# Kernel tuning notes

Hardware: AMD Instinct MI355X
Metric: run time of the kernel (lower is better)

## Reference

```python
import jax, jax.numpy as jnp
import numpy as np

N_PROT, N_LIG = 8192, 2048
E_PP, E_LP = 163840, 81920
D_NODE, D_EDGE, D_CHI = 128, 128, 64
H, DH = 4, 32            # num_attention_heads, head dim (H*DH == D_NODE)
HD = H * DH
D_SRC_PP = 2 * D_NODE + D_EDGE + D_CHI      # 448, pre-expanded pp source feats
Z0 = D_SRC_PP + D_NODE                      # pp edge: [src_exp || prot_sink], edge dim 0
Z1 = 3 * D_NODE                             # lp edge: [lig_src || prot_sink || eattr]
D_FF = 4 * D_NODE


def _ln(x, g, b):
    m = x.mean(-1, keepdims=True)
    v = x.var(-1, keepdims=True)
    return (x - m) / jnp.sqrt(v + 1e-5) * g + b


def _seg_softmax(logits, seg, n):
    # logits: [E, H]; softmax over edges sharing the same sink node
    m = jax.ops.segment_max(logits, seg, num_segments=n)
    e = jnp.exp(logits - m[seg])
    s = jax.ops.segment_sum(e, seg, num_segments=n)
    return e / (s[seg] + 1e-9)


def setup_inputs() -> dict:
    key = jax.random.key(0)
    ks = jax.random.split(key, 32)
    p = lambda k, shape, fan: jax.random.normal(k, shape, jnp.float32) / np.sqrt(fan)
    inp = {
        "source_node_edge_features_exp": jax.random.normal(ks[0], (E_PP, D_SRC_PP), jnp.float32),
        "prot_scalars": jax.random.normal(ks[1], (N_PROT, D_NODE), jnp.float32),
        "prot_vectors": jax.random.normal(ks[2], (N_PROT, 4, 3), jnp.float32),
        "pr_pr_edge_index": jax.random.randint(ks[3], (2, E_PP), 0, N_PROT),
        "lig_scalars": jax.random.normal(ks[4], (N_LIG, D_NODE), jnp.float32),
        "lig_pr_eattr": jax.random.normal(ks[5], (E_LP, D_EDGE), jnp.float32),
        "lig_pr_edge_index": jax.random.randint(ks[6], (2, E_LP), 0, N_LIG),
        # per-edge-type GATv2 weights (subgraph 0 = prot-prot, 1 = lig-prot)
        "Watt0": p(ks[7], (Z0, HD), Z0), "batt0": jnp.zeros((HD,), jnp.float32),
        "a0": p(ks[8], (H, DH), DH),
        "Wval0": p(ks[9], (Z0, HD), Z0), "bval0": jnp.zeros((HD,), jnp.float32),
        "Watt1": p(ks[10], (Z1, HD), Z1), "batt1": jnp.zeros((HD,), jnp.float32),
        "a1": p(ks[11], (H, DH), DH),
        "Wval1": p(ks[12], (Z1, HD), Z1), "bval1": jnp.zeros((HD,), jnp.float32),
        # attention-head aggregation MLP (atten_head_aggr_layers = 2)
        "Wh1": p(ks[13], (HD, HD), HD), "bh1": jnp.zeros((HD,), jnp.float32),
        "Wh2": p(ks[14], (HD, D_NODE), HD), "bh2": jnp.zeros((D_NODE,), jnp.float32),
        "ln1_g": jnp.ones((D_NODE,), jnp.float32), "ln1_b": jnp.zeros((D_NODE,), jnp.float32),
        # residual node-update MLP
        "Wm1": p(ks[15], (D_NODE, D_FF), D_NODE), "bm1": jnp.zeros((D_FF,), jnp.float32),
        "Wm2": p(ks[16], (D_FF, D_NODE), D_FF), "bm2": jnp.zeros((D_NODE,), jnp.float32),
        "ln2_g": jnp.ones((D_NODE,), jnp.float32), "ln2_b": jnp.zeros((D_NODE,), jnp.float32),
    }
    return inp


def reference(source_node_edge_features_exp, prot_scalars, prot_vectors,
              pr_pr_edge_index, lig_scalars, lig_pr_eattr, lig_pr_edge_index,
              Watt0, batt0, a0, Wval0, bval0,
              Watt1, batt1, a1, Wval1, bval1,
              Wh1, bh1, Wh2, bh2, ln1_g, ln1_b,
              Wm1, bm1, Wm2, bm2, ln2_g, ln2_b):
    n = prot_scalars.shape[0]

    def gat(z, sink, Watt, batt, a, Wval, bval):
        e = z.shape[0]
        h = (z @ Watt + batt).reshape(e, H, DH)
        logit = jnp.einsum('ehd,hd->eh', jax.nn.leaky_relu(h, 0.2), a)  # GATv2 scoring
        alpha = _seg_softmax(logit, sink, n)
        v = (z @ Wval + bval).reshape(e, H, DH)
        return jax.ops.segment_sum((v * alpha[..., None]).reshape(e, HD), sink, num_segments=n)

    # gather source/sink features per edge set (pp edges already pre-expanded, edge dim 0)
    z0 = jnp.concatenate([source_node_edge_features_exp, prot_scalars[pr_pr_edge_index[1]]], axis=-1)
    z1 = jnp.concatenate([lig_scalars[lig_pr_edge_index[0]],
                          prot_scalars[lig_pr_edge_index[1]], lig_pr_eattr], axis=-1)
    attn = gat(z0, pr_pr_edge_index[1], Watt0, batt0, a0, Wval0, bval0) \
         + gat(z1, lig_pr_edge_index[1], Watt1, batt1, a1, Wval1, bval1)
    attn = jax.nn.gelu(attn @ Wh1 + bh1) @ Wh2 + bh2       # head aggregation MLP
    x = _ln(prot_scalars + attn, ln1_g, ln1_b)             # residual node update
    x = _ln(x + jax.nn.gelu(x @ Wm1 + bm1) @ Wm2 + bm2, ln2_g, ln2_b)
    return x, prot_vectors  # EquivariantData: updated scalars, vectors pass through
```

## Files before the change

### kernel.cpp

```cpp
#include <hip/hip_runtime.h>

#define N_PROT 8192
#define E_PP   163840
#define E_LP   81920
#define NB0    (E_PP / 64)
#define NB1    (E_LP / 64)
#define XSTR   132

typedef float        f32x2  __attribute__((ext_vector_type(2)));
typedef float        f32x4  __attribute__((ext_vector_type(4)));
typedef float        f32x16 __attribute__((ext_vector_type(16)));
typedef unsigned int u32x2  __attribute__((ext_vector_type(2)));
typedef unsigned int u32x4  __attribute__((ext_vector_type(4)));
typedef short        s16x8  __attribute__((ext_vector_type(8)));
typedef unsigned short ushort_t;

union frag32 { u32x4 v; s16x8 s; };

__device__ inline unsigned short f2bf(float f) {
  unsigned int u = __float_as_uint(f);
  u = u + 0x7FFFu + ((u >> 16) & 1u);
  return (unsigned short)(u >> 16);
}

__device__ inline unsigned int cvt_pk_bf16(float lo, float hi) {
  unsigned int r;
  asm("v_cvt_pk_bf16_f32 %0, %1, %2" : "=v"(r) : "v"(lo), "v"(hi));
  return r;
}

__device__ inline float bf_lo(unsigned int u) { return __uint_as_float(u << 16); }
__device__ inline float bf_hi(unsigned int u) { return __uint_as_float(u & 0xffff0000u); }

__device__ inline float gelu_tanh(float x) {
  const float c0 = 0.7978845608028654f;
  float inner = c0 * (x + 0.044715f * x * x * x);
  return 0.5f * x * (1.0f + tanhf(inner));
}

__global__ void build_bt(const float* __restrict__ Watt, const float* __restrict__ Wval,
                         ushort_t* __restrict__ Bt, int K)
{
  int i = blockIdx.x * 256 + threadIdx.x;
  if (i >= K * 256) return;
  int k = i >> 8, n = i & 255;
  float v = (n < 128) ? Watt[(size_t)k * 128 + n] : Wval[(size_t)k * 128 + (n - 128)];
  Bt[(size_t)(k >> 3) * 2048 + n * 8 + (k & 7)] = f2bf(v);
}

__global__ void build_wt(const float* __restrict__ W, ushort_t* __restrict__ Wt,
                         int total, int shift)
{
  int i = blockIdx.x * 256 + threadIdx.x;
  if (i >= total) return;
  int k = i >> shift, n = i & ((1 << shift) - 1);
  Wt[(size_t)(k >> 3) * (8 << shift) + n * 8 + (k & 7)] = f2bf(W[i]);
}

__global__ void build_perm(const float* __restrict__ batt0, const float* __restrict__ a0,
                           const float* __restrict__ bval0,
                           const float* __restrict__ batt1, const float* __restrict__ a1,
                           const float* __restrict__ bval1,
                           float* __restrict__ P)
{
  const int t = threadIdx.x;
  const int m = t / 384;
  const int r = t % 384;
  const float* batt = m ? batt1 : batt0;
  const float* avec = m ? a1 : a0;
  const float* bval = m ? bval1 : bval0;
  float* base = P + m * 384;
  if (r < 256) {
    const int h = r >> 6, hi = (r >> 5) & 1, q = (r >> 1) & 15, c = r & 1;
    const int rq = (q & 3) + 8 * (q >> 2) + 4 * hi;
    base[r] = c ? avec[h * 32 + rq] : batt[h * 32 + rq];
  } else {
    const int i = r - 256;
    const int g = i >> 5, hi = (i >> 4) & 1, q = i & 15;
    const int rq = (q & 3) + 8 * (q >> 2) + 4 * hi;
    base[256 + i] = bval[g * 32 + rq];
  }
}

__global__ void csr_hist(const int* __restrict__ e0, const int* __restrict__ e1,
                         int* __restrict__ cnt0, int* __restrict__ cnt1)
{
  const int i = blockIdx.x * 256 + threadIdx.x;
  if (i < E_PP) atomicAdd(&cnt0[e0[E_PP + i]], 1);
  if (i < E_LP) atomicAdd(&cnt1[e1[E_LP + i]], 1);
}

__global__ void csr_scan2(const int* __restrict__ cnt0, int* __restrict__ off0,
                          const int* __restrict__ cnt1, int* __restrict__ off1)
{
  const int* cnt = blockIdx.x ? cnt1 : cnt0;
  int* off = blockIdx.x ? off1 : off0;
  __shared__ int ps[1024];
  const int t = threadIdx.x;
  int loc[8];
  int s = 0;
  #pragma unroll
  for (int i = 0; i < 8; ++i) { loc[i] = cnt[t * 8 + i]; s += loc[i]; }
  ps[t] = s;
  __syncthreads();
  for (int d = 1; d < 1024; d <<= 1) {
    int v = (t >= d) ? ps[t - d] : 0;
    __syncthreads();
    ps[t] += v;
    __syncthreads();
  }
  int ex = ps[t] - s;
  #pragma unroll
  for (int i = 0; i < 8; ++i) { off[t * 8 + i] = ex; ex += loc[i]; }
  if (t == 1023) off[8192] = ps[1023];
}

__global__ void csr_scat(const int* __restrict__ e0, const int* __restrict__ e1,
                         const int* __restrict__ off0, const int* __restrict__ off1,
                         int* __restrict__ cur0, int* __restrict__ cur1,
                         int* __restrict__ pel0, int* __restrict__ pel1)
{
  const int i = blockIdx.x * 256 + threadIdx.x;
  if (i < E_PP) { int s = e0[E_PP + i]; pel0[i] = off0[s] + atomicAdd(&cur0[s], 1); }
  if (i < E_LP) { int s = e1[E_LP + i]; pel1[i] = off1[s] + atomicAdd(&cur1[s], 1); }
}

template<int MODE>
__device__ __forceinline__ void edge_body(
    int blk, char* AsmS, char* BsmS, f32x4* epsLds,
    const float* __restrict__ Afeat, const float* __restrict__ prot,
    const float* __restrict__ eattr, const int* __restrict__ eidx,
    const int* __restrict__ pel,
    const ushort_t* __restrict__ Bt, const float* __restrict__ P,
    char* __restrict__ ev, float* __restrict__ eb)
{
  constexpr int K  = (MODE == 0) ? 576 : 384;
  constexpr int E  = (MODE == 0) ? E_PP : E_LP;
  constexpr int NT = K / 16;

  const int t    = threadIdx.x;
  const int lane = t & 63;
  const int w    = t >> 6;
  const int gl   = w >> 1;
  const int role = w & 1;
  const int col  = lane & 31;
  const int hi   = lane >> 5;
  const int eid  = blk * 64 + gl * 32 + col;
  const int pos  = pel[eid];

  const int srow = t >> 2;
  const int sq   = t & 3;
  const int seid = blk * 64 + srow;
  const int ssnk = eidx[E + seid];
  const float* sA;
  const float* sP;
  const float* sE = nullptr;
  if (MODE == 0) {
    sA = Afeat + (size_t)seid * 448 + sq * 4;
    sP = prot  + (size_t)ssnk * 128 + sq * 4;
  } else {
    sA = Afeat + (size_t)eidx[seid] * 128 + sq * 4;
    sP = prot  + (size_t)ssnk * 128 + sq * 4;
    sE = eattr + (size_t)seid * 128 + sq * 4;
  }
  auto sptr = [&](int s) -> const float* {
    const int k0 = s * 16;
    if (MODE == 0) return (k0 < 448) ? (sA + k0) : (sP + (k0 - 448));
    const int r = k0 >> 7, kk = k0 & 127;
    return (r == 0) ? (sA + kk) : (r == 1) ? (sP + kk) : (sE + kk);
  };
  char* const wrA = AsmS + (srow >> 5) * 1536 + (srow & 31) * 48 + sq * 8;
  const char* const rdA = AsmS + gl * 1536 + col * 48 + hi * 16;

  const u32x4* btv = (const u32x4*)Bt;
  char* const wrB = BsmS + t * 32;
  const char* const rdB = BsmS + role * 2048 + hi * 4096 + col * 16;

  f32x16 acc[4];
  #pragma unroll
  for (int i = 0; i < 4; ++i) acc[i] = (f32x16)(0.0f);

  f32x4 gA1, gA2;
  u32x4 gB1a, gB1b, gB2a, gB2b;
  {
    f32x4 g0 = *(const f32x4*)sptr(0);
    u32x4 b0a = btv[t * 2], b0b = btv[t * 2 + 1];
    gA1  = *(const f32x4*)sptr(1);
    gB1a = btv[512 + t * 2];
    gB1b = btv[512 + t * 2 + 1];
    u32x2 pk;
    pk.x = cvt_pk_bf16(g0.x, g0.y);
    pk.y = cvt_pk_bf16(g0.z, g0.w);
    *(u32x2*)wrA = pk;
    u32x4* wb = (u32x4*)wrB;
    wb[0] = b0a; wb[1] = b0b;
  }
  __syncthreads();

  #pragma unroll
  for (int s = 0; s < NT; ++s) {
    const int p = s & 1;
    if (s + 2 < NT) {
      gA2  = *(const f32x4*)sptr(s + 2);
      gB2a = btv[(size_t)(s + 2) * 512 + t * 2];
      gB2b = btv[(size_t)(s + 2) * 512 + t * 2 + 1];
    }

    frag32 af;
    af.v = *(const u32x4*)(rdA + p * 3072);
    const char* bs = rdB + p * 8192;
    #pragma unroll
    for (int nbl = 0; nbl < 4; ++nbl) {
      frag32 bf;
      bf.v = *(const u32x4*)(bs + nbl * 512);
      acc[nbl] = __builtin_amdgcn_mfma_f32_32x32x16_bf16(bf.s, af.s, acc[nbl], 0, 0, 0);
    }

    if (s + 1 < NT) {
      u32x2 pk;
      pk.x = cvt_pk_bf16(gA1.x, gA1.y);
      pk.y = cvt_pk_bf16(gA1.z, gA1.w);
      *(u32x2*)(wrA + (p ^ 1) * 3072) = pk;
      u32x4* wb = (u32x4*)(wrB + (p ^ 1) * 8192);
      wb[0] = gB1a; wb[1] = gB1b;
    }
    gA1 = gA2; gB1a = gB2a; gB1b = gB2b;
    asm volatile("s_waitcnt lgkmcnt(0)\n\ts_barrier" ::: "memory");
  }

  if (role == 0) {
    float ep[4];
    #pragma unroll
    for (int h = 0; h < 4; ++h) {
      const f32x4* tp = (const f32x4*)(P + (h * 2 + hi) * 32);
      float partial = 0.f;
      #pragma unroll
      for (int q = 0; q < 16; q += 2) {
        const f32x4 ba = tp[q >> 1];
        float x0 = acc[h][q]     + ba.x; x0 = (x0 > 0.f) ? x0 : 0.2f * x0;
        float x1 = acc[h][q + 1] + ba.z; x1 = (x1 > 0.f) ? x1 : 0.2f * x1;
        partial = fmaf(x0, ba.y, partial);
        partial = fmaf(x1, ba.w, partial);
      }
      const float full = partial + __shfl_xor(partial, 32, 64);
      ep[h] = __expf(full);
    }
    f32x2 ef2;
    ef2.x = hi ? ep[2] : ep[0];
    ef2.y = hi ? ep[3] : ep[1];
    *(f32x2*)(eb + (size_t)pos * 4 + 2 * hi) = ef2;
    if (hi == 0) {
      f32x4 ef = {ep[0], ep[1], ep[2], ep[3]};
      epsLds[gl * 32 + col] = ef;
    }
  }
  __syncthreads();
  if (role == 1) {
    const f32x4 ep4 = epsLds[gl * 32 + col];
    const float* bvp = P + 256;
    char* row = ev + (size_t)pos * 256;
    #pragma unroll
    for (int g = 0; g < 4; ++g) {
      const float wgt = ep4[g];
      const float* bv = bvp + (g * 2 + hi) * 16;
      #pragma unroll
      for (int s = 0; s < 4; ++s) {
        const float v0 = (acc[g][s * 4 + 0] + bv[s * 4 + 0]) * wgt;
        const float v1 = (acc[g][s * 4 + 1] + bv[s * 4 + 1]) * wgt;
        const float v2 = (acc[g][s * 4 + 2] + bv[s * 4 + 2]) * wgt;
        const float v3 = (acc[g][s * 4 + 3] + bv[s * 4 + 3]) * wgt;
        u32x2 pk;
        pk.x = cvt_pk_bf16(v0, v1);
        pk.y = cvt_pk_bf16(v2, v3);
        *(u32x2*)(row + g * 64 + s * 16 + hi * 8) = pk;
      }
    }
  }
}

__global__ __launch_bounds__(256, 3)
void edge_gat10(const float* __restrict__ src_exp, const float* __restrict__ prot,
                const float* __restrict__ lig, const float* __restrict__ eattr,
                const int* __restrict__ eidx0, const int* __restrict__ eidx1,
                const int* __restrict__ pel0, const int* __restrict__ pel1,
                const ushort_t* __restrict__ Bt0, const ushort_t* __restrict__ Bt1,
                const float* __restrict__ P,
                char* __restrict__ ev0, float* __restrict__ eb0,
                char* __restrict__ ev1, float* __restrict__ eb1)
{
  __shared__ alignas(16) char AsmS[2 * 3072];
  __shared__ alignas(16) char BsmS[2 * 8192];
  __shared__ f32x4 eps[64];
  const int bid = blockIdx.x;
  if (bid < NB0)
    edge_body<0>(bid, AsmS, BsmS, eps, src_exp, prot, nullptr, eidx0, pel0,
                 Bt0, P, ev0, eb0);
  else
    edge_body<1>(bid - NB0, AsmS, BsmS, eps, lig, prot, eattr, eidx1, pel1,
                 Bt1, P + 384, ev1, eb1);
}

__device__ inline void ln_rows16(const float* __restrict__ src, int ss,
                                 float* __restrict__ dst, int ds,
                                 const float* __restrict__ g, const float* __restrict__ b,
                                 const int t)
{
  const int lane = t & 63;
  const int n    = (t >> 6) * 4 + (lane >> 4);
  const int c0   = (lane & 15) * 8;
  f32x4 va = *(const f32x4*)&src[n * ss + c0];
  f32x4 vb = *(const f32x4*)&src[n * ss + c0 + 4];
  float s = va.x + va.y + va.z + va.w + vb.x + vb.y + vb.z + vb.w;
  float q = va.x * va.x + va.y * va.y + va.z * va.z + va.w * va.w
          + vb.x * vb.x + vb.y * vb.y + vb.z * vb.z + vb.w * vb.w;
  #pragma unroll
  for (int m = 1; m < 16; m <<= 1) {
    s += __shfl_xor(s, m, 64);
    q += __shfl_xor(q, m, 64);
  }
  const float mean = s * 0.0078125f;
  const float var  = q * 0.0078125f - mean * mean;
  const float r    = rsqrtf(var + 1e-5f);
  f32x4 oa, ob;
  oa.x = (va.x - mean) * r * g[c0 + 0] + b[c0 + 0];
  oa.y = (va.y - mean) * r * g[c0 + 1] + b[c0 + 1];
  oa.z = (va.z - mean) * r * g[c0 + 2] + b[c0 + 2];
  oa.w = (va.w - mean) * r * g[c0 + 3] + b[c0 + 3];
  ob.x = (vb.x - mean) * r * g[c0 + 4] + b[c0 + 4];
  ob.y = (vb.y - mean) * r * g[c0 + 5] + b[c0 + 5];
  ob.z = (vb.z - mean) * r * g[c0 + 6] + b[c0 + 6];
  ob.w = (vb.w - mean) * r * g[c0 + 7] + b[c0 + 7];
  *(f32x4*)&dst[n * ds + c0]     = oa;
  *(f32x4*)&dst[n * ds + c0 + 4] = ob;
}

__global__ __launch_bounds__(256, 2)
void node_mfma(const int* __restrict__ off0, const char* __restrict__ ev0,
               const float* __restrict__ eb0,
               const int* __restrict__ off1, const char* __restrict__ ev1,
               const float* __restrict__ eb1,
               const float* __restrict__ prot,
               const ushort_t* __restrict__ Wh1t, const float* __restrict__ bh1,
               const ushort_t* __restrict__ Wh2t, const float* __restrict__ bh2,
               const float* __restrict__ ln1g, const float* __restrict__ ln1b,
               const ushort_t* __restrict__ Wm1t, const float* __restrict__ bm1,
               const ushort_t* __restrict__ Wm2t, const float* __restrict__ bm2,
               const float* __restrict__ ln2g, const float* __restrict__ ln2b,
               float* __restrict__ out)
{
  __shared__ alignas(16) char xA[8 * 1536];
  __shared__ alignas(16) char r2[32 * XSTR * 4];
  const int t    = threadIdx.x;
  const int lane = t & 63;
  const int w    = t >> 6;
  const int l31  = lane & 31;
  const int hi   = lane >> 5;
  const int m0   = blockIdx.x * 32;
  float* xs = (float*)r2;
  char*  t3A = r2;

  #pragma unroll
  for (int it = 0; it < 2; ++it) {
    const int u  = t + it * 256;
    const int nl = u >> 4, j = u & 15;
    const int n  = m0 + nl;
    float va0[8] = {0,0,0,0,0,0,0,0}, va1[8] = {0,0,0,0,0,0,0,0};
    float d0v = 0.f, d1v = 0.f;
    {
      const int end = off0[n + 1];
      for (int itr = off0[n]; itr < end; ++itr) {
        const u32x4 r = *(const u32x4*)(ev0 + (size_t)itr * 256 + j * 16);
        d0v += eb0[(size_t)itr * 4 + (j >> 2)];
        #pragma unroll
        for (int i = 0; i < 4; ++i) {
          va0[2 * i]     += bf_lo(r[i]);
          va0[2 * i + 1] += bf_hi(r[i]);
        }
      }
    }
    {
      const int end = off1[n + 1];
      for (int itr = off1[n]; itr < end; ++itr) {
        const u32x4 r = *(const u32x4*)(ev1 + (size_t)itr * 256 + j * 16);
        d1v += eb1[(size_t)itr * 4 + (j >> 2)];
        #pragma unroll
        for (int i = 0; i < 4; ++i) {
          va1[2 * i]     += bf_lo(r[i]);
          va1[2 * i + 1] += bf_hi(r[i]);
        }
      }
    }
    const float inv0 = 1.f / (d0v + 1e-9f);
    const float inv1 = 1.f / (d1v + 1e-9f);
    float res[8];
    #pragma unroll
    for (int i = 0; i < 8; ++i) res[i] = va0[i] * inv0 + va1[i] * inv1;
    u32x4 pk;
    pk.x = cvt_pk_bf16(res[0], res[1]);
    pk.y = cvt_pk_bf16(res[2], res[3]);
    pk.z = cvt_pk_bf16(res[4], res[5]);
    pk.w = cvt_pk_bf16(res[6], res[7]);
    *(u32x4*)(xA + (j >> 1) * 1536 + nl * 48 + (j & 1) * 16) = pk;
  }
  __syncthreads();

  const char* rdA = xA + l31 * 48 + hi * 16;
  f32x16 acc;

  acc = (f32x16)(0.0f);
  #pragma unroll
  for (int s = 0; s < 8; ++s) {
    frag32 af, bf;
    af.v = *(const u32x4*)(rdA + s * 1536);
    bf.v = *(const u32x4*)((const char*)Wh1t + (2 * s + hi) * 2048 + (w * 32 + l31) * 16);
    acc = __builtin_amdgcn_mfma_f32_32x32x16_bf16(bf.s, af.s, acc, 0, 0, 0);
  }
  __syncthreads();
  #pragma unroll
  for (int jr = 0; jr < 4; ++jr) {
    const int c0 = w * 32 + jr * 8 + 4 * hi;
    const f32x4 bb = *(const f32x4*)(bh1 + c0);
    const float v0 = gelu_tanh(acc[4 * jr + 0] + bb.x);
    const float v1 = gelu_tanh(acc[4 * jr + 1] + bb.y);
    const float v2 = gelu_tanh(acc[4 * jr + 2] + bb.z);
    const float v3 = gelu_tanh(acc[4 * jr + 3] + bb.w);
    u32x2 pk;
    pk.x = cvt_pk_bf16(v0, v1);
    pk.y = cvt_pk_bf16(v2, v3);
    *(u32x2*)(xA + (c0 >> 4) * 1536 + l31 * 48 + ((c0 >> 3) & 1) * 16 + (c0 & 7) * 2) = pk;
  }
  __syncthreads();

  acc = (f32x16)(0.0f);
  #pragma unroll
  for (int s = 0; s < 8; ++s) {
    frag32 af, bf;
    af.v = *(const u32x4*)(rdA + s * 1536);
    bf.v = *(const u32x4*)((const char*)Wh2t + (2 * s + hi) * 2048 + (w * 32 + l31) * 16);
    acc = __builtin_amdgcn_mfma_f32_32x32x16_bf16(bf.s, af.s, acc, 0, 0, 0);
  }
  __syncthreads();
  #pragma unroll
  for (int q = 0; q < 16; ++q) {
    const int col = w * 32 + (q & 3) + 8 * (q >> 2) + 4 * hi;
    xs[l31 * XSTR + col] = acc[q];
  }
  __syncthreads();
  #pragma unroll
  for (int it = 0; it < 4; ++it) {
    const int u = t + it * 256;
    const int row = u >> 5, c4 = (u & 31) * 4;
    f32x4 v = *(f32x4*)&xs[row * XSTR + c4];
    const f32x4 p = *(const f32x4*)&prot[(size_t)(m0 + row) * 128 + c4];
    const f32x4 b = *(const f32x4*)&bh2[c4];
    v += p + b;
    *(f32x4*)&xs[row * XSTR + c4] = v;
  }
  __syncthreads();
  ln_rows16(xs, XSTR, xs, XSTR, ln1g, ln1b, t);
  ln_rows16(xs + 16 * XSTR, XSTR, xs + 16 * XSTR, XSTR, ln1g, ln1b, t);
  __syncthreads();
  #pragma unroll
  for (int it = 0; it < 4; ++it) {
    const int u = t + it * 256;
    const int row = u >> 5, c4 = (u & 31) * 4;
    const f32x4 v = *(const f32x4*)&xs[row * XSTR + c4];
    u32x2 pk;
    pk.x = cvt_pk_bf16(v.x, v.y);
    pk.y = cvt_pk_bf16(v.z, v.w);
    *(u32x2*)(xA + (c4 >> 4) * 1536 + row * 48 + ((c4 >> 3) & 1) * 16 + (c4 & 7) * 2) = pk;
  }
  __syncthreads();

  f32x16 acc5 = (f32x16)(0.0f);
  for (int ch = 0; ch < 4; ++ch) {
    f32x16 a4 = (f32x16)(0.0f);
    #pragma unroll
    for (int s = 0; s < 8; ++s) {
      frag32 af, bf;
      af.v = *(const u32x4*)(rdA + s * 1536);
      bf.v = *(const u32x4*)((const char*)Wm1t + (2 * s + hi) * 8192
                             + (ch * 128 + w * 32 + l31) * 16);
      a4 = __builtin_amdgcn_mfma_f32_32x32x16_bf16(bf.s, af.s, a4, 0, 0, 0);
    }
    __syncthreads();
    #pragma unroll
    for (int jr = 0; jr < 4; ++jr) {
      const int c0 = w * 32 + jr * 8 + 4 * hi;
      const f32x4 bb = *(const f32x4*)(bm1 + ch * 128 + c0);
      const float v0 = gelu_tanh(a4[4 * jr + 0] + bb.x);
      const float v1 = gelu_tanh(a4[4 * jr + 1] + bb.y);
      const float v2 = gelu_tanh(a4[4 * jr + 2] + bb.z);
      const float v3 = gelu_tanh(a4[4 * jr + 3] + bb.w);
      u32x2 pk;
      pk.x = cvt_pk_bf16(v0, v1);
      pk.y = cvt_pk_bf16(v2, v3);
      *(u32x2*)(t3A + (c0 >> 4) * 1536 + l31 * 48 + ((c0 >> 3) & 1) * 16 + (c0 & 7) * 2) = pk;
    }
    __syncthreads();
    #pragma unroll
    for (int s = 0; s < 8; ++s) {
      frag32 af, bf;
      af.v = *(const u32x4*)(t3A + s * 1536 + l31 * 48 + hi * 16);
      bf.v = *(const u32x4*)((const char*)Wm2t + (ch * 16 + 2 * s + hi) * 2048
                             + (w * 32 + l31) * 16);
      acc5 = __builtin_amdgcn_mfma_f32_32x32x16_bf16(bf.s, af.s, acc5, 0, 0, 0);
    }
    __syncthreads();
  }

  #pragma unroll
  for (int q = 0; q < 16; ++q) {
    const int col = w * 32 + (q & 3) + 8 * (q >> 2) + 4 * hi;
    xs[l31 * XSTR + col] = acc5[q];
  }
  __syncthreads();
  #pragma unroll
  for (int it = 0; it < 4; ++it) {
    const int u = t + it * 256;
    const int row = u >> 5, c4 = (u & 31) * 4;
    f32x4 v = *(f32x4*)&xs[row * XSTR + c4];
    const u32x2 xx = *(const u32x2*)(xA + (c4 >> 4) * 1536 + row * 48
                                     + ((c4 >> 3) & 1) * 16 + (c4 & 7) * 2);
    const f32x4 b = *(const f32x4*)&bm2[c4];
    v.x += bf_lo(xx.x) + b.x;
    v.y += bf_hi(xx.x) + b.y;
    v.z += bf_lo(xx.y) + b.z;
    v.w += bf_hi(xx.y) + b.w;
    *(f32x4*)&xs[row * XSTR + c4] = v;
  }
  __syncthreads();
  ln_rows16(xs, XSTR, out + (size_t)m0 * 128, 128, ln2g, ln2b, t);
  ln_rows16(xs + 16 * XSTR, XSTR, out + (size_t)(m0 + 16) * 128, 128, ln2g, ln2b, t);
}

extern "C" void kernel_launch(void* const* d_in, const int* in_sizes, int n_in,
                              void* d_out, int out_size, void* d_ws, size_t ws_size,
                              hipStream_t stream)
{
  const float* src_exp = (const float*)d_in[0];
  const float* prot    = (const float*)d_in[1];
  const float* pvec    = (const float*)d_in[2];
  const int*   eidx0   = (const int*)d_in[3];
  const float* lig     = (const float*)d_in[4];
  const float* eattr   = (const float*)d_in[5];
  const int*   eidx1   = (const int*)d_in[6];
  const float* Watt0 = (const float*)d_in[7];
  const float* batt0 = (const float*)d_in[8];
  const float* a0    = (const float*)d_in[9];
  const float* Wval0 = (const float*)d_in[10];
  const float* bval0 = (const float*)d_in[11];
  const float* Watt1 = (const float*)d_in[12];
  const float* batt1 = (const float*)d_in[13];
  const float* a1    = (const float*)d_in[14];
  const float* Wval1 = (const float*)d_in[15];
  const float* bval1 = (const float*)d_in[16];
  const float* Wh1  = (const float*)d_in[17];
  const float* bh1  = (const float*)d_in[18];
  const float* Wh2  = (const float*)d_in[19];
  const float* bh2  = (const float*)d_in[20];
  const float* ln1g = (const float*)d_in[21];
  const float* ln1b = (const float*)d_in[22];
  const float* Wm1  = (const float*)d_in[23];
  const float* bm1  = (const float*)d_in[24];
  const float* Wm2  = (const float*)d_in[25];
  const float* bm2  = (const float*)d_in[26];
  const float* ln2g = (const float*)d_in[27];
  const float* ln2b = (const float*)d_in[28];

  char* w = (char*)d_ws;
  size_t o = 0;
  auto take = [&](size_t b) -> void* {
    void* p = w + o;
    o += (b + 255) & ~(size_t)255;
    return p;
  };
  int* cnt0 = (int*)take(8192 * 4);
  int* cnt1 = (int*)take(8192 * 4);
  int* cur0 = (int*)take(8192 * 4);
  int* cur1 = (int*)take(8192 * 4);
  int* off0 = (int*)take(8193 * 4);
  int* off1 = (int*)take(8193 * 4);
  int* pel0 = (int*)take((size_t)E_PP * 4);
  int* pel1 = (int*)take((size_t)E_LP * 4);
  ushort_t* Bt0 = (ushort_t*)take((size_t)576 * 256 * 2);
  ushort_t* Bt1 = (ushort_t*)take((size_t)384 * 256 * 2);
  ushort_t* Wh1t = (ushort_t*)take((size_t)128 * 128 * 2);
  ushort_t* Wh2t = (ushort_t*)take((size_t)128 * 128 * 2);
  ushort_t* Wm1t = (ushort_t*)take((size_t)128 * 512 * 2);
  ushort_t* Wm2t = (ushort_t*)take((size_t)512 * 128 * 2);
  float* P = (float*)take(768 * 4);
  char*  ev0 = (char*)take((size_t)E_PP * 256);
  char*  ev1 = (char*)take((size_t)E_LP * 256);
  float* eb0 = (float*)take((size_t)E_PP * 16);
  float* eb1 = (float*)take((size_t)E_LP * 16);

  build_bt<<<(576 * 256) / 256, 256, 0, stream>>>(Watt0, Wval0, Bt0, 576);
  build_bt<<<(384 * 256) / 256, 256, 0, stream>>>(Watt1, Wval1, Bt1, 384);
  build_wt<<<64, 256, 0, stream>>>(Wh1, Wh1t, 128 * 128, 7);
  build_wt<<<64, 256, 0, stream>>>(Wh2, Wh2t, 128 * 128, 7);
  build_wt<<<256, 256, 0, stream>>>(Wm1, Wm1t, 128 * 512, 9);
  build_wt<<<256, 256, 0, stream>>>(Wm2, Wm2t, 512 * 128, 7);
  build_perm<<<1, 768, 0, stream>>>(batt0, a0, bval0, batt1, a1, bval1, P);

  hipMemsetAsync(cnt0, 0, 4 * 8192 * 4, stream);
  csr_hist<<<E_PP / 256, 256, 0, stream>>>(eidx0, eidx1, cnt0, cnt1);
  csr_scan2<<<2, 1024, 0, stream>>>(cnt0, off0, cnt1, off1);
  csr_scat<<<E_PP / 256, 256, 0, stream>>>(eidx0, eidx1, off0, off1,
                                           cur0, cur1, pel0, pel1);

  edge_gat10<<<NB0 + NB1, 256, 0, stream>>>(
      src_exp, prot, lig, eattr, eidx0, eidx1, pel0, pel1, Bt0, Bt1, P,
      ev0, eb0, ev1, eb1);

  node_mfma<<<N_PROT / 32, 256, 0, stream>>>(
      off0, ev0, eb0, off1, ev1, eb1, prot,
      Wh1t, bh1, Wh2t, bh2, ln1g, ln1b,
      Wm1t, bm1, Wm2t, bm2, ln2g, ln2b, (float*)d_out);

  hipMemcpyAsync((float*)d_out + (size_t)N_PROT * 128, pvec,
                 (size_t)N_PROT * 12 * sizeof(float), hipMemcpyDeviceToDevice, stream);
}
```

Measured before the change: 289.9 us.

## Split segment gather into a separate high-occupancy kernel and merge prep launches

Moves the per-node CSR aggregation of edge values out of the node MLP kernel into a new seg_gather kernel with 1024 blocks, each node handled by 32 threads that split the edge list in two and combine the halves through shared memory. The result is stored as a bf16 attention buffer that node_mfma then reads. All weight-transposition kernels, the bias permutation and the memset are folded into one prep_all launch to cut launch overhead. The cost is an extra kernel launch and a round trip to global memory for the intermediate buffer.

New measurement: 258.1 us. 11.0% less time.

```diff
diff --git a/kernel.cpp b/kernel.cpp
--- a/kernel.cpp
+++ b/kernel.cpp
@@ -38,47 +38,90 @@
   return 0.5f * x * (1.0f + tanhf(inner));
 }
 
-__global__ void build_bt(const float* __restrict__ Watt, const float* __restrict__ Wval,
-                         ushort_t* __restrict__ Bt, int K)
-{
-  int i = blockIdx.x * 256 + threadIdx.x;
-  if (i >= K * 256) return;
-  int k = i >> 8, n = i & 255;
-  float v = (n < 128) ? Watt[(size_t)k * 128 + n] : Wval[(size_t)k * 128 + (n - 128)];
-  Bt[(size_t)(k >> 3) * 2048 + n * 8 + (k & 7)] = f2bf(v);
-}
-
-__global__ void build_wt(const float* __restrict__ W, ushort_t* __restrict__ Wt,
-                         int total, int shift)
-{
-  int i = blockIdx.x * 256 + threadIdx.x;
-  if (i >= total) return;
-  int k = i >> shift, n = i & ((1 << shift) - 1);
-  Wt[(size_t)(k >> 3) * (8 << shift) + n * 8 + (k & 7)] = f2bf(W[i]);
-}
-
-__global__ void build_perm(const float* __restrict__ batt0, const float* __restrict__ a0,
-                           const float* __restrict__ bval0,
-                           const float* __restrict__ batt1, const float* __restrict__ a1,
-                           const float* __restrict__ bval1,
-                           float* __restrict__ P)
-{
+__global__ void prep_all(const float* __restrict__ Watt0, const float* __restrict__ Wval0,
+                         const float* __restrict__ Watt1, const float* __restrict__ Wval1,
+                         const float* __restrict__ Wh1, const float* __restrict__ Wh2,
+                         const float* __restrict__ Wm1, const float* __restrict__ Wm2,
+                         const float* __restrict__ batt0, const float* __restrict__ a0,
+                         const float* __restrict__ bval0,
+                         const float* __restrict__ batt1, const float* __restrict__ a1,
+                         const float* __restrict__ bval1,
+                         ushort_t* __restrict__ Bt0, ushort_t* __restrict__ Bt1,
+                         ushort_t* __restrict__ Wh1t, ushort_t* __restrict__ Wh2t,
+                         ushort_t* __restrict__ Wm1t, ushort_t* __restrict__ Wm2t,
+                         float* __restrict__ P, int* __restrict__ zbuf)
+{
+  int b = blockIdx.x;
   const int t = threadIdx.x;
-  const int m = t / 384;
-  const int r = t % 384;
-  const float* batt = m ? batt1 : batt0;
-  const float* avec = m ? a1 : a0;
-  const float* bval = m ? bval1 : bval0;
-  float* base = P + m * 384;
-  if (r < 256) {
-    const int h = r >> 6, hi = (r >> 5) & 1, q = (r >> 1) & 15, c = r & 1;
-    const int rq = (q & 3) + 8 * (q >> 2) + 4 * hi;
-    base[r] = c ? avec[h * 32 + rq] : batt[h * 32 + rq];
-  } else {
-    const int i = r - 256;
-    const int g = i >> 5, hi = (i >> 4) & 1, q = i & 15;
-    const int rq = (q & 3) + 8 * (q >> 2) + 4 * hi;
-    base[256 + i] = bval[g * 32 + rq];
+  if (b < 576) {
+    const int i = b * 256 + t;
+    const int k = i >> 8, n = i & 255;
+    const float v = (n < 128) ? Watt0[(size_t)k * 128 + n] : Wval0[(size_t)k * 128 + (n - 128)];
+    Bt0[(size_t)(k >> 3) * 2048 + n * 8 + (k & 7)] = f2bf(v);
+    return;
+  }
+  b -= 576;
+  if (b < 384) {
+    const int i = b * 256 + t;
+    const int k = i >> 8, n = i & 255;
+    const float v = (n < 128) ? Watt1[(size_t)k * 128 + n] : Wval1[(size_t)k * 128 + (n - 128)];
+    Bt1[(size_t)(k >> 3) * 2048 + n * 8 + (k & 7)] = f2bf(v);
+    return;
+  }
+  b -= 384;
+  if (b < 64) {
+    const int i = b * 256 + t;
+    const int k = i >> 7, n = i & 127;
+    Wh1t[(size_t)(k >> 3) * 1024 + n * 8 + (k & 7)] = f2bf(Wh1[i]);
+    return;
+  }
+  b -= 64;
+  if (b < 64) {
+    const int i = b * 256 + t;
+    const int k = i >> 7, n = i & 127;
+    Wh2t[(size_t)(k >> 3) * 1024 + n * 8 + (k & 7)] = f2bf(Wh2[i]);
+    return;
+  }
+  b -= 64;
+  if (b < 256) {
+    const int i = b * 256 + t;
+    const int k = i >> 9, n = i & 511;
+    Wm1t[(size_t)(k >> 3) * 4096 + n * 8 + (k & 7)] = f2bf(Wm1[i]);
+    return;
+  }
+  b -= 256;
+  if (b < 256) {
+    const int i = b * 256 + t;
+    const int k = i >> 7, n = i & 127;
+    Wm2t[(size_t)(k >> 3) * 1024 + n * 8 + (k & 7)] = f2bf(Wm2[i]);
+    return;
+  }
+  b -= 256;
+  if (b < 3) {
+    const int u = b * 256 + t;
+    if (u >= 768) return;
+    const int m = u / 384;
+    const int r = u % 384;
+    const float* batt = m ? batt1 : batt0;
+    const float* avec = m ? a1 : a0;
+    const float* bval = m ? bval1 : bval0;
+    float* base = P + m * 384;
+    if (r < 256) {
+      const int h = r >> 6, hi = (r >> 5) & 1, q = (r >> 1) & 15, c = r & 1;
+      const int rq = (q & 3) + 8 * (q >> 2) + 4 * hi;
+      base[r] = c ? avec[h * 32 + rq] : batt[h * 32 + rq];
+    } else {
+      const int i = r - 256;
+      const int g = i >> 5, hi = (i >> 4) & 1, q = i & 15;
+      const int rq = (q & 3) + 8 * (q >> 2) + 4 * hi;
+      base[256 + i] = bval[g * 32 + rq];
+    }
+    return;
+  }
+  b -= 3;
+  {
+    const int i = b * 256 + t;
+    if (i < 32768) zbuf[i] = 0;
   }
 }
 
@@ -300,6 +343,71 @@
                  Bt1, P + 384, ev1, eb1);
 }
 
+__global__ __launch_bounds__(256)
+void seg_gather(const int* __restrict__ off0, const char* __restrict__ ev0,
+                const float* __restrict__ eb0,
+                const int* __restrict__ off1, const char* __restrict__ ev1,
+                const float* __restrict__ eb1,
+                ushort_t* __restrict__ att)
+{
+  __shared__ float xch[8 * 16 * 18];
+  const int t    = threadIdx.x;
+  const int nl   = t >> 5;
+  const int half = (t >> 4) & 1;
+  const int j    = t & 15;
+  const int n    = blockIdx.x * 8 + nl;
+
+  float va0[8] = {0,0,0,0,0,0,0,0}, va1[8] = {0,0,0,0,0,0,0,0};
+  float d0 = 0.f, d1 = 0.f;
+  {
+    const int end = off0[n + 1];
+    for (int it = off0[n] + half; it < end; it += 2) {
+      const u32x4 r = *(const u32x4*)(ev0 + (size_t)it * 256 + j * 16);
+      d0 += eb0[(size_t)it * 4 + (j >> 2)];
+      #pragma unroll
+      for (int i = 0; i < 4; ++i) {
+        va0[2 * i]     += bf_lo(r[i]);
+        va0[2 * i + 1] += bf_hi(r[i]);
+      }
+    }
+  }
+  {
+    const int end = off1[n + 1];
+    for (int it = off1[n] + half; it < end; it += 2) {
+      const u32x4 r = *(const u32x4*)(ev1 + (size_t)it * 256 + j * 16);
+      d1 += eb1[(size_t)it * 4 + (j >> 2)];
+      #pragma unroll
+      for (int i = 0; i < 4; ++i) {
+        va1[2 * i]     += bf_lo(r[i]);
+        va1[2 * i + 1] += bf_hi(r[i]);
+      }
+    }
+  }
+  float* slot = xch + (nl * 16 + j) * 18;
+  if (half) {
+    #pragma unroll
+    for (int i = 0; i < 8; ++i) { slot[i] = va0[i]; slot[8 + i] = va1[i]; }
+    slot[16] = d0; slot[17] = d1;
+  }
+  __syncthreads();
+  if (!half) {
+    #pragma unroll
+    for (int i = 0; i < 8; ++i) { va0[i] += slot[i]; va1[i] += slot[8 + i]; }
+    d0 += slot[16]; d1 += slot[17];
+    const float inv0 = 1.f / (d0 + 1e-9f);
+    const float inv1 = 1.f / (d1 + 1e-9f);
+    float res[8];
+    #pragma unroll
+    for (int i = 0; i < 8; ++i) res[i] = va0[i] * inv0 + va1[i] * inv1;
+    u32x4 pk;
+    pk.x = cvt_pk_bf16(res[0], res[1]);
+    pk.y = cvt_pk_bf16(res[2], res[3]);
+    pk.z = cvt_pk_bf16(res[4], res[5]);
+    pk.w = cvt_pk_bf16(res[6], res[7]);
+    *(u32x4*)(att + (size_t)n * 128 + j * 8) = pk;
+  }
+}
+
 __device__ inline void ln_rows16(const float* __restrict__ src, int ss,
                                  float* __restrict__ dst, int ds,
                                  const float* __restrict__ g, const float* __restrict__ b,
@@ -335,10 +443,7 @@
 }
 
 __global__ __launch_bounds__(256, 2)
-void node_mfma(const int* __restrict__ off0, const char* __restrict__ ev0,
-               const float* __restrict__ eb0,
-               const int* __restrict__ off1, const char* __restrict__ ev1,
-               const float* __restrict__ eb1,
+void node_mfma(const ushort_t* __restrict__ att,
                const float* __restrict__ prot,
                const ushort_t* __restrict__ Wh1t, const float* __restrict__ bh1,
                const ushort_t* __restrict__ Wh2t, const float* __restrict__ bh2,
@@ -363,43 +468,7 @@
   for (int it = 0; it < 2; ++it) {
     const int u  = t + it * 256;
     const int nl = u >> 4, j = u & 15;
-    const int n  = m0 + nl;
-    float va0[8] = {0,0,0,0,0,0,0,0}, va1[8] = {0,0,0,0,0,0,0,0};
-    float d0v = 0.f, d1v = 0.f;
-    {
-      const int end = off0[n + 1];
-      for (int itr = off0[n]; itr < end; ++itr) {
-        const u32x4 r = *(const u32x4*)(ev0 + (size_t)itr * 256 + j * 16);
-        d0v += eb0[(size_t)itr * 4 + (j >> 2)];
-        #pragma unroll
-        for (int i = 0; i < 4; ++i) {
-          va0[2 * i]     += bf_lo(r[i]);
-          va0[2 * i + 1] += bf_hi(r[i]);
-        }
-      }
-    }
-    {
-      const int end = off1[n + 1];
-      for (int itr = off1[n]; itr < end; ++itr) {
-        const u32x4 r = *(const u32x4*)(ev1 + (size_t)itr * 256 + j * 16);
-        d1v += eb1[(size_t)itr * 4 + (j >> 2)];
-        #pragma unroll
-        for (int i = 0; i < 4; ++i) {
-          va1[2 * i]     += bf_lo(r[i]);
-          va1[2 * i + 1] += bf_hi(r[i]);
-        }
-      }
-    }
-    const float inv0 = 1.f / (d0v + 1e-9f);
-    const float inv1 = 1.f / (d1v + 1e-9f);
-    float res[8];
-    #pragma unroll
-    for (int i = 0; i < 8; ++i) res[i] = va0[i] * inv0 + va1[i] * inv1;
-    u32x4 pk;
-    pk.x = cvt_pk_bf16(res[0], res[1]);
-    pk.y = cvt_pk_bf16(res[2], res[3]);
-    pk.z = cvt_pk_bf16(res[4], res[5]);
-    pk.w = cvt_pk_bf16(res[6], res[7]);
+    const u32x4 pk = *(const u32x4*)(att + (size_t)(m0 + nl) * 128 + j * 8);
     *(u32x4*)(xA + (j >> 1) * 1536 + nl * 48 + (j & 1) * 16) = pk;
   }
   __syncthreads();
@@ -590,20 +659,17 @@
   ushort_t* Wm1t = (ushort_t*)take((size_t)128 * 512 * 2);
   ushort_t* Wm2t = (ushort_t*)take((size_t)512 * 128 * 2);
   float* P = (float*)take(768 * 4);
+  ushort_t* att = (ushort_t*)take((size_t)N_PROT * 128 * 2);
   char*  ev0 = (char*)take((size_t)E_PP * 256);
   char*  ev1 = (char*)take((size_t)E_LP * 256);
   float* eb0 = (float*)take((size_t)E_PP * 16);
   float* eb1 = (float*)take((size_t)E_LP * 16);
 
-  build_bt<<<(576 * 256) / 256, 256, 0, stream>>>(Watt0, Wval0, Bt0, 576);
-  build_bt<<<(384 * 256) / 256, 256, 0, stream>>>(Watt1, Wval1, Bt1, 384);
-  build_wt<<<64, 256, 0, stream>>>(Wh1, Wh1t, 128 * 128, 7);
-  build_wt<<<64, 256, 0, stream>>>(Wh2, Wh2t, 128 * 128, 7);
-  build_wt<<<256, 256, 0, stream>>>(Wm1, Wm1t, 128 * 512, 9);
-  build_wt<<<256, 256, 0, stream>>>(Wm2, Wm2t, 512 * 128, 7);
-  build_perm<<<1, 768, 0, stream>>>(batt0, a0, bval0, batt1, a1, bval1, P);
-
-  hipMemsetAsync(cnt0, 0, 4 * 8192 * 4, stream);
+  prep_all<<<1731, 256, 0, stream>>>(Watt0, Wval0, Watt1, Wval1,
+                                     Wh1, Wh2, Wm1, Wm2,
+                                     batt0, a0, bval0, batt1, a1, bval1,
+                                     Bt0, Bt1, Wh1t, Wh2t, Wm1t, Wm2t, P, cnt0);
+
   csr_hist<<<E_PP / 256, 256, 0, stream>>>(eidx0, eidx1, cnt0, cnt1);
   csr_scan2<<<2, 1024, 0, stream>>>(cnt0, off0, cnt1, off1);
   csr_scat<<<E_PP / 256, 256, 0, stream>>>(eidx0, eidx1, off0, off1,
@@ -613,8 +679,10 @@
       src_exp, prot, lig, eattr, eidx0, eidx1, pel0, pel1, Bt0, Bt1, P,
       ev0, eb0, ev1, eb1);
 
+  seg_gather<<<N_PROT / 8, 256, 0, stream>>>(off0, ev0, eb0, off1, ev1, eb1, att);
+
   node_mfma<<<N_PROT / 32, 256, 0, stream>>>(
-      off0, ev0, eb0, off1, ev1, eb1, prot,
+      att, prot,
       Wh1t, bh1, Wh2t, bh2, ln1g, ln1b,
       Wm1t, bm1, Wm2t, bm2, ln2g, ln2b, (float*)d_out);
 
```
